# Kernel tuning notes

Hardware: AMD Instinct MI355X
Metric: run time of the kernel (lower is better)

The kernel has to match this reference:

```python
import jax, jax.numpy as jnp
import numpy as np

T, B, DIN, H, AA, L = 1024, 32, 256, 256, 21, 2


def setup_inputs() -> dict:
    key = jax.random.key(0)
    ks = jax.random.split(key, 8)
    scale = 0.05

    def rn(i, shape):
        return jax.random.normal(ks[i], shape, dtype=jnp.float32) * scale

    return {
        "x": jax.random.normal(ks[0], (B, T, DIN), dtype=jnp.float32),
        "hidden": jnp.zeros((2 * L, B, H), jnp.float32),  # accepted but unused, as in torch forward
        # layer 0: input DIN -> per-direction 4 chunks of H; layer 1: input 2H
        "w_l0": rn(1, (DIN, 2, 4, H)),
        "wc_l0": rn(2, (2, 2, H)),            # [dir, (v_f, v_r), H]
        "b_l0": jnp.zeros((2, 2, H), jnp.float32),  # [dir, (b_f, b_r), H]
        "w_l1": rn(3, (2 * H, 2, 4, H)),
        "wc_l1": rn(4, (2, 2, H)),
        "b_l1": jnp.zeros((2, 2, H), jnp.float32),
        "fc1_w": rn(5, (H, 2 * H)),
        "fc1_b": jnp.zeros((H,), jnp.float32),
        "lp_w": rn(6, (AA, H)),
        "lp_b": jnp.zeros((AA,), jnp.float32),
    }


def _sru_scan(u, vf, vr, bf, br):
    # u: (T, B, 4, H) with chunks [candidate, forget, reset, highway]
    def step(c, ut):
        f = jax.nn.sigmoid(ut[:, 1] + vf * c + bf)
        c2 = f * c + (1.0 - f) * ut[:, 0]
        r = jax.nn.sigmoid(ut[:, 2] + vr * c + br)
        h = r * c2 + (1.0 - r) * ut[:, 3]
        return c2, h

    c0 = jnp.zeros((u.shape[1], u.shape[-1]), u.dtype)
    _, hs = jax.lax.scan(step, c0, u)
    return hs  # (T, B, H)


def _sru_layer(x, w, wc, b):
    # x: (T, B, Din); w: (Din, 2, 4, H)
    U = jnp.einsum('tbd,dnkh->tbnkh', x, w)
    hf = _sru_scan(U[:, :, 0], wc[0, 0], wc[0, 1], b[0, 0], b[0, 1])
    hb = _sru_scan(U[::-1, :, 1], wc[1, 0], wc[1, 1], b[1, 0], b[1, 1])[::-1]
    return jnp.concatenate([hf, hb], axis=-1)  # (T, B, 2H)


def reference(x, hidden, w_l0, wc_l0, b_l0, w_l1, wc_l1, b_l1, fc1_w, fc1_b, lp_w, lp_b):
    h = jnp.transpose(x, (1, 0, 2))  # (T, B, DIN)
    h = _sru_layer(h, w_l0, wc_l0, b_l0)
    h = _sru_layer(h, w_l1, wc_l1, b_l1)
    h = jnp.transpose(h, (1, 0, 2))  # (B, T, 2H)
    h = h @ fc1_w.T + fc1_b
    logits = h @ lp_w.T + lp_b
    return jax.nn.log_softmax(logits, axis=-1)  # (B, T, AA)
```

## Files before the change

kernel.cpp:

```cpp
#include <hip/hip_runtime.h>
#include <hip/hip_bf16.h>

#define T_DIM 1024
#define B_DIM 32
#define DIN_DIM 256
#define H_DIM 256
#define AA_DIM 21
#define M_ROWS (B_DIM * T_DIM)

typedef __attribute__((ext_vector_type(8))) short bf16x8;
typedef __attribute__((ext_vector_type(4))) float f32x4;

typedef __attribute__((address_space(3))) void lds_void;
typedef const __attribute__((address_space(1))) void glb_void;

#define LOG2E_F 1.44269504088896340736f

__device__ __forceinline__ void gload_lds16(const void* g, void* l) {
    __builtin_amdgcn_global_load_lds((glb_void*)g, (lds_void*)l, 16, 0, 0);
}

__device__ __forceinline__ float b2f(unsigned short v) {
    unsigned u = ((unsigned)v) << 16;
    float f;
    __builtin_memcpy(&f, &u, 4);
    return f;
}

__device__ __forceinline__ unsigned short f2bu(float f) {
    __hip_bfloat16 h = __float2bfloat16(f);
    unsigned short u;
    __builtin_memcpy(&u, &h, 2);
    return u;
}

#define CVT_V0 2097152
#define CVT_N1 524288
#define CVT_N2 1048576
#define CVT_V3 32768
#define CVT_N4 8192
#define CVT_TOT (CVT_V0 + CVT_N1 + CVT_N2 + CVT_V3 + CVT_N4)
__global__ __launch_bounds__(256) void cvt_all(
    const float* __restrict__ x,  const float* __restrict__ w0,
    const float* __restrict__ w1, const float* __restrict__ fcw,
    const float* __restrict__ lpw,
    __hip_bfloat16* __restrict__ xb,  __hip_bfloat16* __restrict__ w0t,
    __hip_bfloat16* __restrict__ w1t, __hip_bfloat16* __restrict__ fcwb,
    __hip_bfloat16* __restrict__ lpwb)
{
    int i = blockIdx.x * 256 + threadIdx.x;
    if (i < CVT_V0) {
        float4 v = ((const float4*)x)[i];
        ushort4 o = { f2bu(v.x), f2bu(v.y), f2bu(v.z), f2bu(v.w) };
        ((ushort4*)xb)[i] = o;
        return;
    }
    i -= CVT_V0;
    if (i < CVT_N1) {
        int kk = i >> 11, rem = i & 2047;
        int dir = rem >> 10, k = (rem >> 8) & 3, h = rem & 255;
        w0t[(long)(dir * 1024 + h * 4 + k) * 256 + kk] = __float2bfloat16(w0[i]);
        return;
    }
    i -= CVT_N1;
    if (i < CVT_N2) {
        int kk = i >> 11, rem = i & 2047;
        int dir = rem >> 10, k = (rem >> 8) & 3, h = rem & 255;
        w1t[(long)(dir * 1024 + h * 4 + k) * 512 + kk] = __float2bfloat16(w1[i]);
        return;
    }
    i -= CVT_N2;
    if (i < CVT_V3) {
        float4 v = ((const float4*)fcw)[i];
        ushort4 o = { f2bu(v.x), f2bu(v.y), f2bu(v.z), f2bu(v.w) };
        ((ushort4*)fcwb)[i] = o;
        return;
    }
    i -= CVT_V3;
    if (i < CVT_N4) {
        int n = i >> 8, k = i & 255;
        lpwb[i] = __float2bfloat16(n < AA_DIM ? lpw[n * 256 + k] : 0.0f);
    }
}

template<int U2OUT>
__global__ __launch_bounds__(256) void gemm_bf16(
    const __hip_bfloat16* __restrict__ A,
    const __hip_bfloat16* __restrict__ Bt,
    const float* __restrict__ bias,
    __hip_bfloat16* __restrict__ C,
    int M, int N, int K, int nbShift)
{
    __shared__ __align__(16) char smb[32768];

    const int tid  = threadIdx.x;
    const int lane = tid & 63;
    const int wave = tid >> 6;
    const int wm = wave & 1;
    const int wn = wave >> 1;

    const int L   = blockIdx.x;
    const int s   = L >> 3;
    const int nb  = s & ((1 << nbShift) - 1);
    const int mb  = ((s >> nbShift) << 3) + (L & 7);
    const long n0 = (long)nb * 128;
    const long m0 = (long)mb * 128;

    f32x4 acc[4][4] = {};

    const int ldrow = lane >> 2;
    const int ldq   = lane & 3;
    const int gq    = ldq ^ ((ldrow >> 1) & 3);
    const int gkoff = gq * 8;

    const int fr = lane & 15;
    const int kq = lane >> 4;
    const int sw = (kq ^ ((fr >> 1) & 3)) * 16;

    for (int kb = 0; kb < K; kb += 64) {
        __syncthreads();
#pragma unroll
        for (int i = 0; i < 4; ++i) {
            const int cid = wave * 4 + i;
            const int rc  = cid >> 1;
            const int kh  = cid & 1;
            const long row = rc * 16 + ldrow;
            const int koff = kb + kh * 32 + gkoff;
            gload_lds16(A  + (m0 + row) * (long)K + koff,
                        smb + rc * 2048 + kh * 1024);
            gload_lds16(Bt + (n0 + row) * (long)K + koff,
                        smb + 16384 + rc * 2048 + kh * 1024);
        }
        __syncthreads();

#pragma unroll
        for (int ss = 0; ss < 2; ++ss) {
            bf16x8 af[4], bfv[4];
#pragma unroll
            for (int i = 0; i < 4; ++i) {
                af[i]  = *(const bf16x8*)(smb + (wm * 4 + i) * 2048 + ss * 1024 + fr * 64 + sw);
                bfv[i] = *(const bf16x8*)(smb + 16384 + (wn * 4 + i) * 2048 + ss * 1024 + fr * 64 + sw);
            }
#pragma unroll
            for (int i = 0; i < 4; ++i)
#pragma unroll
                for (int j = 0; j < 4; ++j)
                    acc[i][j] = __builtin_amdgcn_mfma_f32_16x16x32_bf16(
                        af[i], bfv[j], acc[i][j], 0, 0, 0);
        }
    }

    const int col_l = lane & 15;
    const int row_l = (lane >> 4) * 4;
    __hip_bfloat16* smC = (__hip_bfloat16*)smb;
#pragma unroll
    for (int p = 0; p < 2; ++p) {
        __syncthreads();
        if (wm == p) {
#pragma unroll
            for (int j = 0; j < 4; ++j) {
                const long gc = n0 + wn * 64 + j * 16 + col_l;
                const float bv = bias ? bias[gc] : 0.0f;
#pragma unroll
                for (int i = 0; i < 4; ++i)
#pragma unroll
                    for (int r = 0; r < 4; ++r)
                        smC[(i * 16 + row_l + r) * 132 + wn * 64 + j * 16 + col_l] =
                            __float2bfloat16(acc[i][j][r] + bv);
            }
        }
        __syncthreads();
        const int cb = (tid & 7) * 16;
#pragma unroll
        for (int s2 = 0; s2 < 2; ++s2) {
            const int rr = s2 * 32 + (tid >> 3);
            const long gr = m0 + p * 64 + rr;
            bf16x8 v0 = *(const bf16x8*)(smC + rr * 132 + cb);
            bf16x8 v1 = *(const bf16x8*)(smC + rr * 132 + cb + 8);
            if (U2OUT) {
                const int bI  = (int)(gr >> 10);
                const int t   = (int)(gr & 1023);
                const long gc0 = n0 + cb;
                const int dir = (int)(gc0 >> 10);
                const int hg  = ((int)gc0 >> 8) & 3;
                const int beta = bI * 8 + dir * 4 + hg;
                const long base = ((long)beta * 1024 + t) * 256 + (gc0 & 255);
                *(bf16x8*)(C + base)     = v0;
                *(bf16x8*)(C + base + 8) = v1;
            } else {
                *(bf16x8*)(C + gr * (long)N + n0 + cb)     = v0;
                *(bf16x8*)(C + gr * (long)N + n0 + cb + 8) = v1;
            }
        }
    }
}

#define SCAN_S 64
#define SCAN_NB (T_DIM / SCAN_S)
#define GRP 16

__device__ __forceinline__ float scan_step(
    uint2 u, float c, float nvf, float nvr, float nbf, float nbr,
    __hip_bfloat16* hq)
{
    float u0, u1, u2, u3;
    unsigned a0 = u.x << 16, a1 = u.x & 0xffff0000u;
    unsigned a2 = u.y << 16, a3 = u.y & 0xffff0000u;
    __builtin_memcpy(&u0, &a0, 4); __builtin_memcpy(&u1, &a1, 4);
    __builtin_memcpy(&u2, &a2, 4); __builtin_memcpy(&u3, &a3, 4);
    const float nf0 = __builtin_fmaf(-LOG2E_F, u1, nbf);
    const float nr0 = __builtin_fmaf(-LOG2E_F, u2, nbr);
    const float ef = __builtin_amdgcn_exp2f(__builtin_fmaf(nvf, c, nf0));
    const float er = __builtin_amdgcn_exp2f(__builtin_fmaf(nvr, c, nr0));
    const float f  = __builtin_amdgcn_rcpf(1.0f + ef);
    const float r  = __builtin_amdgcn_rcpf(1.0f + er);
    const float c2 = __builtin_fmaf(f, c - u0, u0);
    const float hv = __builtin_fmaf(r, c2 - u3, u3);
    *hq = __float2bfloat16(hv);
    return c2;
}

__global__ __launch_bounds__(256) void sru_scan(
    const __hip_bfloat16* __restrict__ U2,
    const float* __restrict__ wc,
    const float* __restrict__ bias,
    __hip_bfloat16* __restrict__ hout)
{
    __shared__ __align__(16) char lds[2 * SCAN_S * 512];
    const int tid  = threadIdx.x;
    const int wave = tid >> 6;
    const int lane = tid & 63;
    const int beta = blockIdx.x;
    const int b    = beta >> 3;
    const int dir  = (beta >> 2) & 1;
    const int hg   = beta & 3;
    const int h    = hg * 64 + lane;

    const char* gslice = (const char*)U2 + (size_t)beta * (1024 * 512);

    const float nvf = -LOG2E_F * wc[(dir * 2 + 0) * H_DIM + h];
    const float nvr = -LOG2E_F * wc[(dir * 2 + 1) * H_DIM + h];
    const float nbf = -LOG2E_F * bias[(dir * 2 + 0) * H_DIM + h];
    const float nbr = -LOG2E_F * bias[(dir * 2 + 1) * H_DIM + h];
    __hip_bfloat16* hp = hout + ((long)(b * 1024 + (dir ? 1023 : 0))) * 512 + dir * 256 + h;
    const long hstep = dir ? -512L : 512L;
    float c = 0.0f;

    const int plane = lane & 31;

    if (wave > 0) {
        for (int p = wave - 1; p < SCAN_S / 2; p += 3) {
            const int sl = 2 * p + (lane >> 5);
            const int t  = dir ? (1023 - sl) : sl;
            gload_lds16(gslice + (size_t)t * 512 + plane * 16, lds + p * 1024);
        }
    }
    __syncthreads();

    for (int bat = 0; bat < SCAN_NB; ++bat) {
        if (wave > 0) {
            if (bat + 1 < SCAN_NB) {
                char* halfN = lds + ((bat + 1) & 1) * (SCAN_S * 512);
                const int tb = (bat + 1) * SCAN_S;
                for (int p = wave - 1; p < SCAN_S / 2; p += 3) {
                    const int sl = tb + 2 * p + (lane >> 5);
                    const int t  = dir ? (1023 - sl) : sl;
                    gload_lds16(gslice + (size_t)t * 512 + plane * 16,
                                halfN + p * 1024);
                }
            }
        } else {
            const char* half = lds + (bat & 1) * (SCAN_S * 512);
            __hip_bfloat16* hq = hp + (long)(bat * SCAN_S) * hstep;
            uint2 qa[GRP], qb[GRP];
#pragma unroll
            for (int j = 0; j < GRP; ++j)
                qa[j] = *(const uint2*)(half + (0 * GRP + j) * 512 + (lane << 3));
#pragma unroll
            for (int j = 0; j < GRP; ++j)
                qb[j] = *(const uint2*)(half + (1 * GRP + j) * 512 + (lane << 3));
#pragma unroll
            for (int j = 0; j < GRP; ++j)
                c = scan_step(qa[j], c, nvf, nvr, nbf, nbr, hq + (long)j * hstep);
#pragma unroll
            for (int j = 0; j < GRP; ++j)
                qa[j] = *(const uint2*)(half + (2 * GRP + j) * 512 + (lane << 3));
#pragma unroll
            for (int j = 0; j < GRP; ++j)
                c = scan_step(qb[j], c, nvf, nvr, nbf, nbr, hq + (long)(GRP + j) * hstep);
#pragma unroll
            for (int j = 0; j < GRP; ++j)
                qb[j] = *(const uint2*)(half + (3 * GRP + j) * 512 + (lane << 3));
#pragma unroll
            for (int j = 0; j < GRP; ++j)
                c = scan_step(qa[j], c, nvf, nvr, nbf, nbr, hq + (long)(2 * GRP + j) * hstep);
#pragma unroll
            for (int j = 0; j < GRP; ++j)
                c = scan_step(qb[j], c, nvf, nvr, nbf, nbr, hq + (long)(3 * GRP + j) * hstep);
        }
        __syncthreads();
    }
}

__global__ __launch_bounds__(256) void logits_mfma(
    const __hip_bfloat16* __restrict__ fc,
    const __hip_bfloat16* __restrict__ lpwb,
    const float* __restrict__ lpb,
    float* __restrict__ out)
{
    __shared__ __align__(16) char smb[25088];
    const int tid  = threadIdx.x;
    const int lane = tid & 63;
    const int wave = tid >> 6;
    const long m0  = (long)blockIdx.x * 128;

    for (int idx = tid; idx < 32 * 32; idx += 256) {
        const int rw = idx >> 5, sl = idx & 31;
        *(bf16x8*)(smb + rw * 528 + sl * 16) =
            *(const bf16x8*)(lpwb + rw * 256 + sl * 8);
    }

    const int ldrow = lane >> 2;
    const int ldq   = lane & 3;
    const int gq    = ldq ^ ((ldrow >> 1) & 3);
    const int gkoff = gq * 8;

    const int fr = lane & 15;
    const int kq = lane >> 4;
    const int sw = (kq ^ ((fr >> 1) & 3)) * 16;

    f32x4 acc[2][2] = {};
    for (int kc = 0; kc < 8; ++kc) {
        __syncthreads();
#pragma unroll
        for (int i = 0; i < 2; ++i) {
            const int rc = wave * 2 + i;
            gload_lds16(fc + (m0 + rc * 16 + ldrow) * 256 + kc * 32 + gkoff,
                        smb + 16896 + rc * 1024);
        }
        __syncthreads();
        bf16x8 af[2], bfv[2];
#pragma unroll
        for (int i = 0; i < 2; ++i)
            af[i] = *(const bf16x8*)(smb + 16896 + (wave * 2 + i) * 1024 + fr * 64 + sw);
#pragma unroll
        for (int j = 0; j < 2; ++j)
            bfv[j] = *(const bf16x8*)(smb + (j * 16 + fr) * 528 + kc * 64 + kq * 16);
#pragma unroll
        for (int i = 0; i < 2; ++i)
#pragma unroll
            for (int j = 0; j < 2; ++j)
                acc[i][j] = __builtin_amdgcn_mfma_f32_16x16x32_bf16(
                    af[i], bfv[j], acc[i][j], 0, 0, 0);
    }

    __syncthreads();
    float* smC = (float*)smb;
    const int col_l = lane & 15;
    const int row_l = (lane >> 4) * 4;
#pragma unroll
    for (int j = 0; j < 2; ++j) {
        const int gc = j * 16 + col_l;
        const float bv = (gc < AA_DIM) ? lpb[gc] : 0.0f;
#pragma unroll
        for (int i = 0; i < 2; ++i)
#pragma unroll
            for (int r = 0; r < 4; ++r)
                smC[(wave * 32 + i * 16 + row_l + r) * 36 + gc] = acc[i][j][r] + bv;
    }
    __syncthreads();
    if (tid < 128) {
        const float* rowp = smC + tid * 36;
        float m = rowp[0];
#pragma unroll
        for (int a = 1; a < AA_DIM; ++a) m = fmaxf(m, rowp[a]);
        float s = 0.0f;
#pragma unroll
        for (int a = 0; a < AA_DIM; ++a) s += __expf(rowp[a] - m);
        const float lse = __logf(s) + m;
        float* op = out + (m0 + tid) * AA_DIM;
#pragma unroll
        for (int a = 0; a < AA_DIM; ++a) op[a] = rowp[a] - lse;
    }
}

extern "C" void kernel_launch(void* const* d_in, const int* in_sizes, int n_in,
                              void* d_out, int out_size, void* d_ws, size_t ws_size,
                              hipStream_t stream)
{
    const float* x     = (const float*)d_in[0];
    const float* w_l0  = (const float*)d_in[2];
    const float* wc_l0 = (const float*)d_in[3];
    const float* b_l0  = (const float*)d_in[4];
    const float* w_l1  = (const float*)d_in[5];
    const float* wc_l1 = (const float*)d_in[6];
    const float* b_l1  = (const float*)d_in[7];
    const float* fc1_w = (const float*)d_in[8];
    const float* fc1_b = (const float*)d_in[9];
    const float* lp_w  = (const float*)d_in[10];
    const float* lp_b  = (const float*)d_in[11];
    float* out = (float*)d_out;

    char* ws = (char*)d_ws;
    __hip_bfloat16* U      = (__hip_bfloat16*)(ws);
    __hip_bfloat16* h0b    = (__hip_bfloat16*)(ws + 134217728);
    __hip_bfloat16* h1b    = (__hip_bfloat16*)(ws + 167772160);
    __hip_bfloat16* xb     = (__hip_bfloat16*)(ws + 201326592);
    __hip_bfloat16* fcob   = xb;
    __hip_bfloat16* w0t    = (__hip_bfloat16*)(ws + 218103808);
    __hip_bfloat16* w1t    = (__hip_bfloat16*)(ws + 219152384);
    __hip_bfloat16* fc1wb  = (__hip_bfloat16*)(ws + 221249536);
    __hip_bfloat16* lpwb   = (__hip_bfloat16*)(ws + 221511680);

    cvt_all<<<(CVT_TOT + 255) / 256, 256, 0, stream>>>(
        x, w_l0, w_l1, fc1_w, lp_w, xb, w0t, w1t, fc1wb, lpwb);

    gemm_bf16<1><<<4096, 256, 0, stream>>>(
        xb, w0t, nullptr, U, M_ROWS, 2048, DIN_DIM, 4);
    sru_scan<<<256, 256, 0, stream>>>(U, wc_l0, b_l0, h0b);
    gemm_bf16<1><<<4096, 256, 0, stream>>>(
        h0b, w1t, nullptr, U, M_ROWS, 2048, 512, 4);
    sru_scan<<<256, 256, 0, stream>>>(U, wc_l1, b_l1, h1b);
    gemm_bf16<0><<<512, 256, 0, stream>>>(
        h1b, fc1wb, fc1_b, fcob, M_ROWS, 256, 512, 1);
    logits_mfma<<<M_ROWS / 128, 256, 0, stream>>>(fcob, lpwb, lp_b, out);
}
```

Measured before the change: 402.2 us.

## Add 256x256-tile double-buffered MFMA GEMM for SRU input projections

Replaces the two large U-projection GEMMs with a new 512-thread kernel that computes 256x256 output tiles. It double-buffers K-tiles in 128KB of LDS through direct global-to-LDS loads and interleaves LDS fragment reads with MFMA bursts under barriers and raised wave priority. Larger tiles raise arithmetic intensity and cut redundant A/B loads. The cost is high LDS and register use per block, which limits occupancy, and the epilogue now writes the permuted U layout through an LDS staging buffer.

```diff
diff --git a/kernel.cpp b/kernel.cpp
--- a/kernel.cpp
+++ b/kernel.cpp
@@ -80,6 +80,176 @@
     if (i < CVT_N4) {
         int n = i >> 8, k = i & 255;
         lpwb[i] = __float2bfloat16(n < AA_DIM ? lpw[n * 256 + k] : 0.0f);
+    }
+}
+
+__device__ __forceinline__ void stage_tile256(
+    const __hip_bfloat16* __restrict__ A,
+    const __hip_bfloat16* __restrict__ Bt,
+    char* buf, long m0, long n0, int K, int kb,
+    int wave, int ldrow, int gkoff)
+{
+#pragma unroll
+    for (int i = 0; i < 4; ++i) {
+        const int cid = wave * 4 + i;
+        const int rc  = cid >> 1;
+        const int kh  = cid & 1;
+        const long row = rc * 16 + ldrow;
+        const int koff = kb + kh * 32 + gkoff;
+        gload_lds16(A  + (m0 + row) * (long)K + koff,
+                    buf + rc * 2048 + kh * 1024);
+        gload_lds16(Bt + (n0 + row) * (long)K + koff,
+                    buf + 32768 + rc * 2048 + kh * 1024);
+    }
+}
+
+#define MFMA16(d, a, b) d = __builtin_amdgcn_mfma_f32_16x16x32_bf16(a, b, d, 0, 0, 0)
+
+__global__ __launch_bounds__(512, 2) void gemm256_u2(
+    const __hip_bfloat16* __restrict__ A,
+    const __hip_bfloat16* __restrict__ Bt,
+    __hip_bfloat16* __restrict__ C,
+    int K, int nbShift)
+{
+    __shared__ __align__(16) char smb[131072];
+
+    const int tid  = threadIdx.x;
+    const int lane = tid & 63;
+    const int wave = tid >> 6;
+    const int wm   = wave >> 2;
+    const int wn   = wave & 3;
+
+    const int L  = blockIdx.x;
+    const int s  = L >> 3;
+    const int nb = s & ((1 << nbShift) - 1);
+    const int mb = ((s >> nbShift) << 3) + (L & 7);
+    const long n0 = (long)nb * 256;
+    const long m0 = (long)mb * 256;
+
+    const int ldrow = lane >> 2;
+    const int ldq   = lane & 3;
+    const int gq    = ldq ^ ((ldrow >> 1) & 3);
+    const int gkoff = gq * 8;
+
+    const int fr = lane & 15;
+    const int kq = lane >> 4;
+    const int sw = (kq ^ ((fr >> 1) & 3)) * 16;
+
+    f32x4 acc[8][4] = {};
+    const int NT = K >> 6;
+
+    stage_tile256(A, Bt, smb,         m0, n0, K, 0,  wave, ldrow, gkoff);
+    __builtin_amdgcn_sched_barrier(0);
+    stage_tile256(A, Bt, smb + 65536, m0, n0, K, 64, wave, ldrow, gkoff);
+    asm volatile("s_waitcnt vmcnt(8)" ::: "memory");
+    __builtin_amdgcn_s_barrier();
+
+    for (int kt = 0; kt < NT; ++kt) {
+        char* rb = smb + (kt & 1) * 65536;
+        const char* Ab = rb + (wm * 8) * 2048;
+        const char* Bb = rb + 32768 + (wn * 4) * 2048;
+        bf16x8 a0[4], a1[4], bv[4];
+
+#pragma unroll
+        for (int i = 0; i < 4; ++i) {
+            a0[i] = *(const bf16x8*)(Ab + i * 2048 + fr * 64 + sw);
+            bv[i] = *(const bf16x8*)(Bb + i * 2048 + fr * 64 + sw);
+        }
+        __builtin_amdgcn_s_barrier();
+        __builtin_amdgcn_s_setprio(1);
+#pragma unroll
+        for (int i = 0; i < 4; ++i)
+#pragma unroll
+            for (int j = 0; j < 4; ++j)
+                MFMA16(acc[i][j], a0[i], bv[j]);
+        __builtin_amdgcn_s_setprio(0);
+        __builtin_amdgcn_s_barrier();
+
+#pragma unroll
+        for (int i = 0; i < 4; ++i)
+            a1[i] = *(const bf16x8*)(Ab + (4 + i) * 2048 + fr * 64 + sw);
+        __builtin_amdgcn_s_barrier();
+        __builtin_amdgcn_s_setprio(1);
+#pragma unroll
+        for (int i = 0; i < 4; ++i)
+#pragma unroll
+            for (int j = 0; j < 4; ++j)
+                MFMA16(acc[4 + i][j], a1[i], bv[j]);
+        __builtin_amdgcn_s_setprio(0);
+        __builtin_amdgcn_s_barrier();
+
+#pragma unroll
+        for (int i = 0; i < 4; ++i) {
+            a0[i] = *(const bf16x8*)(Ab + i * 2048 + 1024 + fr * 64 + sw);
+            bv[i] = *(const bf16x8*)(Bb + i * 2048 + 1024 + fr * 64 + sw);
+        }
+        __builtin_amdgcn_s_barrier();
+        __builtin_amdgcn_s_setprio(1);
+#pragma unroll
+        for (int i = 0; i < 4; ++i)
+#pragma unroll
+            for (int j = 0; j < 4; ++j)
+                MFMA16(acc[i][j], a0[i], bv[j]);
+        __builtin_amdgcn_s_setprio(0);
+        __builtin_amdgcn_s_barrier();
+
+#pragma unroll
+        for (int i = 0; i < 4; ++i)
+            a1[i] = *(const bf16x8*)(Ab + (4 + i) * 2048 + 1024 + fr * 64 + sw);
+        __builtin_amdgcn_s_barrier();
+        __builtin_amdgcn_s_setprio(1);
+#pragma unroll
+        for (int i = 0; i < 4; ++i)
+#pragma unroll
+            for (int j = 0; j < 4; ++j)
+                MFMA16(acc[4 + i][j], a1[i], bv[j]);
+        __builtin_amdgcn_s_setprio(0);
+        __builtin_amdgcn_s_barrier();
+
+        __builtin_amdgcn_sched_barrier(0);
+        if (kt + 2 < NT) {
+            stage_tile256(A, Bt, rb, m0, n0, K, (kt + 2) * 64,
+                          wave, ldrow, gkoff);
+            asm volatile("s_waitcnt vmcnt(8)" ::: "memory");
+        } else if (kt + 1 < NT) {
+            asm volatile("s_waitcnt vmcnt(0)" ::: "memory");
+        }
+        __builtin_amdgcn_s_barrier();
+    }
+
+    const int col_l = lane & 15;
+    const int row_l = (lane >> 4) * 4;
+    __hip_bfloat16* smC = (__hip_bfloat16*)smb;
+    const int chunk = tid & 31;
+    const int rbase = tid >> 5;
+#pragma unroll
+    for (int p = 0; p < 2; ++p) {
+        __syncthreads();
+        if (wm == p) {
+#pragma unroll
+            for (int i = 0; i < 8; ++i)
+#pragma unroll
+                for (int j = 0; j < 4; ++j)
+#pragma unroll
+                    for (int r = 0; r < 4; ++r)
+                        smC[(i * 16 + row_l + r) * 264 + wn * 64 + j * 16 + col_l] =
+                            __float2bfloat16(acc[i][j][r]);
+        }
+        __syncthreads();
+#pragma unroll
+        for (int it = 0; it < 8; ++it) {
+            const int rr = it * 16 + rbase;
+            bf16x8 v = *(const bf16x8*)(smC + rr * 264 + chunk * 8);
+            const long gr  = m0 + p * 128 + rr;
+            const long gc0 = n0 + chunk * 8;
+            const int bI  = (int)(gr >> 10);
+            const int t   = (int)(gr & 1023);
+            const int dir = (int)(gc0 >> 10);
+            const int hg  = ((int)gc0 >> 8) & 3;
+            const int beta = bI * 8 + dir * 4 + hg;
+            const long base = ((long)beta * 1024 + t) * 256 + ((int)gc0 & 255);
+            *(bf16x8*)(C + base) = v;
+        }
     }
 }
 
@@ -415,11 +585,9 @@
     cvt_all<<<(CVT_TOT + 255) / 256, 256, 0, stream>>>(
         x, w_l0, w_l1, fc1_w, lp_w, xb, w0t, w1t, fc1wb, lpwb);
 
-    gemm_bf16<1><<<4096, 256, 0, stream>>>(
-        xb, w0t, nullptr, U, M_ROWS, 2048, DIN_DIM, 4);
+    gemm256_u2<<<1024, 512, 0, stream>>>(xb, w0t, U, DIN_DIM, 3);
     sru_scan<<<256, 256, 0, stream>>>(U, wc_l0, b_l0, h0b);
-    gemm_bf16<1><<<4096, 256, 0, stream>>>(
-        h0b, w1t, nullptr, U, M_ROWS, 2048, 512, 4);
+    gemm256_u2<<<1024, 512, 0, stream>>>(h0b, w1t, U, 512, 3);
     sru_scan<<<256, 256, 0, stream>>>(U, wc_l1, b_l1, h1b);
     gemm_bf16<0><<<512, 256, 0, stream>>>(
         h1b, fc1wb, fc1_b, fcob, M_ROWS, 256, 512, 1);
```

After: 389.1 us. 1.03x faster.

## Fuse SRU input projection GEMM with recurrent scan in warp-specialized kernel

Applied to the files above, without the earlier changes.

Replaces the separate projection GEMM and scan kernels for each layer with one kernel. Eight producer waves compute 64-timestep chunks of U with MFMA into double-buffered LDS, and one consumer wave runs the recurrence from LDS. This removes the round trip of the large U intermediate through global memory and overlaps the matmul with the sequential scan. The cost is that the GEMM now runs on only 256 blocks with one block per CU, and correctness depends on hand-written barrier and waitcnt synchronization.

```diff
diff --git a/kernel.cpp b/kernel.cpp
--- a/kernel.cpp
+++ b/kernel.cpp
@@ -18,13 +18,6 @@
 
 __device__ __forceinline__ void gload_lds16(const void* g, void* l) {
     __builtin_amdgcn_global_load_lds((glb_void*)g, (lds_void*)l, 16, 0, 0);
-}
-
-__device__ __forceinline__ float b2f(unsigned short v) {
-    unsigned u = ((unsigned)v) << 16;
-    float f;
-    __builtin_memcpy(&f, &u, 4);
-    return f;
 }
 
 __device__ __forceinline__ unsigned short f2bu(float f) {
@@ -83,6 +76,203 @@
     }
 }
 
+#define MFMA16(d, a, b) d = __builtin_amdgcn_mfma_f32_16x16x32_bf16(a, b, d, 0, 0, 0)
+
+__device__ __forceinline__ float scan_step(
+    uint2 u, float c, float nvf, float nvr, float nbf, float nbr,
+    __hip_bfloat16* hq)
+{
+    float u0, u1, u2, u3;
+    unsigned a0 = u.x << 16, a1 = u.x & 0xffff0000u;
+    unsigned a2 = u.y << 16, a3 = u.y & 0xffff0000u;
+    __builtin_memcpy(&u0, &a0, 4); __builtin_memcpy(&u1, &a1, 4);
+    __builtin_memcpy(&u2, &a2, 4); __builtin_memcpy(&u3, &a3, 4);
+    const float nf0 = __builtin_fmaf(-LOG2E_F, u1, nbf);
+    const float nr0 = __builtin_fmaf(-LOG2E_F, u2, nbr);
+    const float ef = __builtin_amdgcn_exp2f(__builtin_fmaf(nvf, c, nf0));
+    const float er = __builtin_amdgcn_exp2f(__builtin_fmaf(nvr, c, nr0));
+    const float f  = __builtin_amdgcn_rcpf(1.0f + ef);
+    const float r  = __builtin_amdgcn_rcpf(1.0f + er);
+    const float c2 = __builtin_fmaf(f, c - u0, u0);
+    const float hv = __builtin_fmaf(r, c2 - u3, u3);
+    *hq = __float2bfloat16(hv);
+    return c2;
+}
+
+#define CH_S 64
+#define NCH (T_DIM / CH_S)
+#define USTRIDE 520
+#define UBUF_SZ (CH_S * USTRIDE)
+#define BOFF (2 * UBUF_SZ)
+#define LDS_TOT (BOFF + 8 * 2 * 4096)
+
+template<int K>
+__global__ __launch_bounds__(576, 1) void fused_sru(
+    const __hip_bfloat16* __restrict__ A,
+    const __hip_bfloat16* __restrict__ Bt,
+    const float* __restrict__ wc,
+    const float* __restrict__ bias,
+    __hip_bfloat16* __restrict__ hout)
+{
+    constexpr int NK = K / 64;
+    __shared__ __align__(16) char lds[LDS_TOT];
+
+    const int tid  = threadIdx.x;
+    const int wave = tid >> 6;
+    const int lane = tid & 63;
+    const int beta = blockIdx.x;
+    const int b    = beta >> 3;
+    const int dir  = (beta >> 2) & 1;
+    const int hg   = beta & 3;
+
+    if (wave < 8) {
+        const int fr = lane & 15, kq = lane >> 4;
+        const int sw = (kq ^ ((fr >> 1) & 3)) * 16;
+        const int ldrow = lane >> 2, ldq = lane & 3;
+        const int gq = ldq ^ ((ldrow >> 1) & 3);
+        const int gkoff = gq * 8;
+        char* bb = lds + BOFF + wave * 8192;
+        const int nb0 = dir * 1024 + hg * 256;
+        const long arowB = (long)b * 1024;
+        const long browW = (long)(nb0 + wave * 32);
+        const int row_l = (lane >> 4) * 4;
+        const int col_l = lane & 15;
+
+        bf16x8 ar[2][8];
+
+        {
+            const long arow0 = arowB + (dir ? (1024 - CH_S) : 0);
+#pragma unroll
+            for (int g = 0; g < 2; ++g) {
+#pragma unroll
+                for (int i = 0; i < 4; ++i)
+#pragma unroll
+                    for (int kh = 0; kh < 2; ++kh)
+                        ar[g][i * 2 + kh] = *(const bf16x8*)(A +
+                            (arow0 + i * 16 + fr) * (long)K + g * 64 + kh * 32 + kq * 8);
+#pragma unroll
+                for (int j = 0; j < 2; ++j)
+#pragma unroll
+                    for (int kh = 0; kh < 2; ++kh)
+                        gload_lds16(Bt + (browW + j * 16 + ldrow) * (long)K +
+                                        g * 64 + kh * 32 + gkoff,
+                                    bb + g * 4096 + j * 2048 + kh * 1024);
+                __builtin_amdgcn_sched_barrier(0);
+            }
+        }
+
+        for (int c = 0; c < NCH; ++c) {
+            const long arow_c = arowB + (dir ? (long)(1024 - (c + 1) * CH_S)
+                                             : (long)(c * CH_S));
+            const long arow_n = arowB + (dir ? (long)(1024 - (c + 2) * CH_S)
+                                             : (long)((c + 1) * CH_S));
+            const bool haveN = (c + 1 < NCH);
+            f32x4 acc[4][2] = {};
+            __hip_bfloat16* ub = (__hip_bfloat16*)(lds + (c & 1) * UBUF_SZ);
+
+#pragma unroll
+            for (int ks = 0; ks < NK; ++ks) {
+                if (c == NCH - 1 && ks == NK - 1)
+                    asm volatile("s_waitcnt vmcnt(0)" ::: "memory");
+                else
+                    asm volatile("s_waitcnt vmcnt(12)" ::: "memory");
+
+                bf16x8 bfr[4];
+#pragma unroll
+                for (int j = 0; j < 2; ++j)
+#pragma unroll
+                    for (int kh = 0; kh < 2; ++kh)
+                        bfr[j * 2 + kh] = *(const bf16x8*)(bb + (ks & 1) * 4096 +
+                                           j * 2048 + kh * 1024 + fr * 64 + sw);
+#pragma unroll
+                for (int kh = 0; kh < 2; ++kh)
+#pragma unroll
+                    for (int i = 0; i < 4; ++i)
+#pragma unroll
+                        for (int j = 0; j < 2; ++j)
+                            MFMA16(acc[i][j], ar[ks & 1][i * 2 + kh], bfr[j * 2 + kh]);
+
+                const bool wrap = (ks + 2 >= NK);
+                const int  nks  = wrap ? (ks + 2 - NK) : (ks + 2);
+                const long arw  = wrap ? arow_n : arow_c;
+                if (!wrap || haveN) {
+#pragma unroll
+                    for (int i = 0; i < 4; ++i)
+#pragma unroll
+                        for (int kh = 0; kh < 2; ++kh)
+                            ar[ks & 1][i * 2 + kh] = *(const bf16x8*)(A +
+                                (arw + i * 16 + fr) * (long)K + nks * 64 + kh * 32 + kq * 8);
+#pragma unroll
+                    for (int j = 0; j < 2; ++j)
+#pragma unroll
+                        for (int kh = 0; kh < 2; ++kh)
+                            gload_lds16(Bt + (browW + j * 16 + ldrow) * (long)K +
+                                            nks * 64 + kh * 32 + gkoff,
+                                        bb + (ks & 1) * 4096 + j * 2048 + kh * 1024);
+                }
+            }
+
+#pragma unroll
+            for (int i = 0; i < 4; ++i)
+#pragma unroll
+                for (int j = 0; j < 2; ++j)
+#pragma unroll
+                    for (int r = 0; r < 4; ++r)
+                        ub[(i * 16 + row_l + r) * (USTRIDE / 2) +
+                           wave * 32 + j * 16 + col_l] =
+                            __float2bfloat16(acc[i][j][r]);
+
+            asm volatile("s_waitcnt lgkmcnt(0)" ::: "memory");
+            __builtin_amdgcn_s_barrier();
+            asm volatile("" ::: "memory");
+            __builtin_amdgcn_sched_barrier(0);
+        }
+    } else {
+        const int h = hg * 64 + lane;
+        const float nvf = -LOG2E_F * wc[(dir * 2 + 0) * H_DIM + h];
+        const float nvr = -LOG2E_F * wc[(dir * 2 + 1) * H_DIM + h];
+        const float nbf = -LOG2E_F * bias[(dir * 2 + 0) * H_DIM + h];
+        const float nbr = -LOG2E_F * bias[(dir * 2 + 1) * H_DIM + h];
+        __hip_bfloat16* hp = hout + ((long)(b * 1024 + (dir ? 1023 : 0))) * 512 +
+                             dir * 256 + h;
+        const long hstep = dir ? -512L : 512L;
+        float cc = 0.0f;
+
+        for (int c = 0; c < NCH; ++c) {
+            __builtin_amdgcn_s_barrier();
+            asm volatile("" ::: "memory");
+            __builtin_amdgcn_sched_barrier(0);
+            const char* ub = lds + (c & 1) * UBUF_SZ;
+            __hip_bfloat16* hq = hp + (long)(c * CH_S) * hstep;
+            uint2 qa[16], qb[16];
+#pragma unroll
+            for (int j = 0; j < 16; ++j)
+                qa[j] = *(const uint2*)(ub + (dir ? (63 - j) : j) * USTRIDE + (lane << 3));
+#pragma unroll
+            for (int j = 0; j < 16; ++j)
+                qb[j] = *(const uint2*)(ub + (dir ? (47 - j) : (16 + j)) * USTRIDE + (lane << 3));
+#pragma unroll
+            for (int j = 0; j < 16; ++j)
+                cc = scan_step(qa[j], cc, nvf, nvr, nbf, nbr, hq + (long)j * hstep);
+#pragma unroll
+            for (int j = 0; j < 16; ++j)
+                qa[j] = *(const uint2*)(ub + (dir ? (31 - j) : (32 + j)) * USTRIDE + (lane << 3));
+#pragma unroll
+            for (int j = 0; j < 16; ++j)
+                cc = scan_step(qb[j], cc, nvf, nvr, nbf, nbr, hq + (long)(16 + j) * hstep);
+#pragma unroll
+            for (int j = 0; j < 16; ++j)
+                qb[j] = *(const uint2*)(ub + (dir ? (15 - j) : (48 + j)) * USTRIDE + (lane << 3));
+#pragma unroll
+            for (int j = 0; j < 16; ++j)
+                cc = scan_step(qa[j], cc, nvf, nvr, nbf, nbr, hq + (long)(32 + j) * hstep);
+#pragma unroll
+            for (int j = 0; j < 16; ++j)
+                cc = scan_step(qb[j], cc, nvf, nvr, nbf, nbr, hq + (long)(48 + j) * hstep);
+        }
+    }
+}
+
 template<int U2OUT>
 __global__ __launch_bounds__(256) void gemm_bf16(
     const __hip_bfloat16* __restrict__ A,
@@ -195,113 +385,6 @@
     }
 }
 
-#define SCAN_S 64
-#define SCAN_NB (T_DIM / SCAN_S)
-#define GRP 16
-
-__device__ __forceinline__ float scan_step(
-    uint2 u, float c, float nvf, float nvr, float nbf, float nbr,
-    __hip_bfloat16* hq)
-{
-    float u0, u1, u2, u3;
-    unsigned a0 = u.x << 16, a1 = u.x & 0xffff0000u;
-    unsigned a2 = u.y << 16, a3 = u.y & 0xffff0000u;
-    __builtin_memcpy(&u0, &a0, 4); __builtin_memcpy(&u1, &a1, 4);
-    __builtin_memcpy(&u2, &a2, 4); __builtin_memcpy(&u3, &a3, 4);
-    const float nf0 = __builtin_fmaf(-LOG2E_F, u1, nbf);
-    const float nr0 = __builtin_fmaf(-LOG2E_F, u2, nbr);
-    const float ef = __builtin_amdgcn_exp2f(__builtin_fmaf(nvf, c, nf0));
-    const float er = __builtin_amdgcn_exp2f(__builtin_fmaf(nvr, c, nr0));
-    const float f  = __builtin_amdgcn_rcpf(1.0f + ef);
-    const float r  = __builtin_amdgcn_rcpf(1.0f + er);
-    const float c2 = __builtin_fmaf(f, c - u0, u0);
-    const float hv = __builtin_fmaf(r, c2 - u3, u3);
-    *hq = __float2bfloat16(hv);
-    return c2;
-}
-
-__global__ __launch_bounds__(256) void sru_scan(
-    const __hip_bfloat16* __restrict__ U2,
-    const float* __restrict__ wc,
-    const float* __restrict__ bias,
-    __hip_bfloat16* __restrict__ hout)
-{
-    __shared__ __align__(16) char lds[2 * SCAN_S * 512];
-    const int tid  = threadIdx.x;
-    const int wave = tid >> 6;
-    const int lane = tid & 63;
-    const int beta = blockIdx.x;
-    const int b    = beta >> 3;
-    const int dir  = (beta >> 2) & 1;
-    const int hg   = beta & 3;
-    const int h    = hg * 64 + lane;
-
-    const char* gslice = (const char*)U2 + (size_t)beta * (1024 * 512);
-
-    const float nvf = -LOG2E_F * wc[(dir * 2 + 0) * H_DIM + h];
-    const float nvr = -LOG2E_F * wc[(dir * 2 + 1) * H_DIM + h];
-    const float nbf = -LOG2E_F * bias[(dir * 2 + 0) * H_DIM + h];
-    const float nbr = -LOG2E_F * bias[(dir * 2 + 1) * H_DIM + h];
-    __hip_bfloat16* hp = hout + ((long)(b * 1024 + (dir ? 1023 : 0))) * 512 + dir * 256 + h;
-    const long hstep = dir ? -512L : 512L;
-    float c = 0.0f;
-
-    const int plane = lane & 31;
-
-    if (wave > 0) {
-        for (int p = wave - 1; p < SCAN_S / 2; p += 3) {
-            const int sl = 2 * p + (lane >> 5);
-            const int t  = dir ? (1023 - sl) : sl;
-            gload_lds16(gslice + (size_t)t * 512 + plane * 16, lds + p * 1024);
-        }
-    }
-    __syncthreads();
-
-    for (int bat = 0; bat < SCAN_NB; ++bat) {
-        if (wave > 0) {
-            if (bat + 1 < SCAN_NB) {
-                char* halfN = lds + ((bat + 1) & 1) * (SCAN_S * 512);
-                const int tb = (bat + 1) * SCAN_S;
-                for (int p = wave - 1; p < SCAN_S / 2; p += 3) {
-                    const int sl = tb + 2 * p + (lane >> 5);
-                    const int t  = dir ? (1023 - sl) : sl;
-                    gload_lds16(gslice + (size_t)t * 512 + plane * 16,
-                                halfN + p * 1024);
-                }
-            }
-        } else {
-            const char* half = lds + (bat & 1) * (SCAN_S * 512);
-            __hip_bfloat16* hq = hp + (long)(bat * SCAN_S) * hstep;
-            uint2 qa[GRP], qb[GRP];
-#pragma unroll
-            for (int j = 0; j < GRP; ++j)
-                qa[j] = *(const uint2*)(half + (0 * GRP + j) * 512 + (lane << 3));
-#pragma unroll
-            for (int j = 0; j < GRP; ++j)
-                qb[j] = *(const uint2*)(half + (1 * GRP + j) * 512 + (lane << 3));
-#pragma unroll
-            for (int j = 0; j < GRP; ++j)
-                c = scan_step(qa[j], c, nvf, nvr, nbf, nbr, hq + (long)j * hstep);
-#pragma unroll
-            for (int j = 0; j < GRP; ++j)
-                qa[j] = *(const uint2*)(half + (2 * GRP + j) * 512 + (lane << 3));
-#pragma unroll
-            for (int j = 0; j < GRP; ++j)
-                c = scan_step(qb[j], c, nvf, nvr, nbf, nbr, hq + (long)(GRP + j) * hstep);
-#pragma unroll
-            for (int j = 0; j < GRP; ++j)
-                qb[j] = *(const uint2*)(half + (3 * GRP + j) * 512 + (lane << 3));
-#pragma unroll
-            for (int j = 0; j < GRP; ++j)
-                c = scan_step(qa[j], c, nvf, nvr, nbf, nbr, hq + (long)(2 * GRP + j) * hstep);
-#pragma unroll
-            for (int j = 0; j < GRP; ++j)
-                c = scan_step(qb[j], c, nvf, nvr, nbf, nbr, hq + (long)(3 * GRP + j) * hstep);
-        }
-        __syncthreads();
-    }
-}
-
 __global__ __launch_bounds__(256) void logits_mfma(
     const __hip_bfloat16* __restrict__ fc,
     const __hip_bfloat16* __restrict__ lpwb,
@@ -402,7 +485,6 @@
     float* out = (float*)d_out;
 
     char* ws = (char*)d_ws;
-    __hip_bfloat16* U      = (__hip_bfloat16*)(ws);
     __hip_bfloat16* h0b    = (__hip_bfloat16*)(ws + 134217728);
     __hip_bfloat16* h1b    = (__hip_bfloat16*)(ws + 167772160);
     __hip_bfloat16* xb     = (__hip_bfloat16*)(ws + 201326592);
@@ -415,12 +497,9 @@
     cvt_all<<<(CVT_TOT + 255) / 256, 256, 0, stream>>>(
         x, w_l0, w_l1, fc1_w, lp_w, xb, w0t, w1t, fc1wb, lpwb);
 
-    gemm_bf16<1><<<4096, 256, 0, stream>>>(
-        xb, w0t, nullptr, U, M_ROWS, 2048, DIN_DIM, 4);
-    sru_scan<<<256, 256, 0, stream>>>(U, wc_l0, b_l0, h0b);
-    gemm_bf16<1><<<4096, 256, 0, stream>>>(
-        h0b, w1t, nullptr, U, M_ROWS, 2048, 512, 4);
-    sru_scan<<<256, 256, 0, stream>>>(U, wc_l1, b_l1, h1b);
+    fused_sru<256><<<256, 576, 0, stream>>>(xb,  w0t, wc_l0, b_l0, h0b);
+    fused_sru<512><<<256, 576, 0, stream>>>(h0b, w1t, wc_l1, b_l1, h1b);
+
     gemm_bf16<0><<<512, 256, 0, stream>>>(
         h1b, fc1wb, fc1_b, fcob, M_ROWS, 256, 512, 1);
     logits_mfma<<<M_ROWS / 128, 256, 0, stream>>>(fcob, lpwb, lp_b, out);
```

Result: slower. 566.7 us (+40.9%).

## Double-buffer LDS tiles in bf16 GEMM to overlap global loads with MFMA

Applied to the files above, without the earlier changes.

The GEMM kernel now keeps two 32 KB LDS stages. It issues the async global-to-LDS loads for tile k+1 before computing tile k, and uses a manual vmcnt wait with raw s_barrier in place of two __syncthreads per iteration. It also raises wave priority around the MFMA block and requests two blocks per CU through launch bounds. This aims to hide global load latency behind matrix math, at the cost of doubling LDS use to 64 KB per block, which may limit occupancy. The K loops are short (4 or 8 tiles), so the prologue load is exposed for a relatively large share of each block.

```diff
diff --git a/kernel.cpp b/kernel.cpp
--- a/kernel.cpp
+++ b/kernel.cpp
@@ -18,13 +18,6 @@
 
 __device__ __forceinline__ void gload_lds16(const void* g, void* l) {
     __builtin_amdgcn_global_load_lds((glb_void*)g, (lds_void*)l, 16, 0, 0);
-}
-
-__device__ __forceinline__ float b2f(unsigned short v) {
-    unsigned u = ((unsigned)v) << 16;
-    float f;
-    __builtin_memcpy(&f, &u, 4);
-    return f;
 }
 
 __device__ __forceinline__ unsigned short f2bu(float f) {
@@ -83,15 +76,17 @@
     }
 }
 
+#define MFMA16(d, a, b) d = __builtin_amdgcn_mfma_f32_16x16x32_bf16(a, b, d, 0, 0, 0)
+
 template<int U2OUT>
-__global__ __launch_bounds__(256) void gemm_bf16(
+__global__ __launch_bounds__(256, 2) void gemm128_db(
     const __hip_bfloat16* __restrict__ A,
     const __hip_bfloat16* __restrict__ Bt,
     const float* __restrict__ bias,
     __hip_bfloat16* __restrict__ C,
     int M, int N, int K, int nbShift)
 {
-    __shared__ __align__(16) char smb[32768];
+    __shared__ __align__(16) char smb[65536];
 
     const int tid  = threadIdx.x;
     const int lane = tid & 63;
@@ -117,38 +112,59 @@
     const int kq = lane >> 4;
     const int sw = (kq ^ ((fr >> 1) & 3)) * 16;
 
-    for (int kb = 0; kb < K; kb += 64) {
-        __syncthreads();
-#pragma unroll
-        for (int i = 0; i < 4; ++i) {
-            const int cid = wave * 4 + i;
-            const int rc  = cid >> 1;
-            const int kh  = cid & 1;
-            const long row = rc * 16 + ldrow;
-            const int koff = kb + kh * 32 + gkoff;
-            gload_lds16(A  + (m0 + row) * (long)K + koff,
-                        smb + rc * 2048 + kh * 1024);
-            gload_lds16(Bt + (n0 + row) * (long)K + koff,
-                        smb + 16384 + rc * 2048 + kh * 1024);
-        }
-        __syncthreads();
+    const int NT = K >> 6;
+
+#define STAGE128(BUF, KB)                                                   \
+    do {                                                                    \
+        _Pragma("unroll")                                                   \
+        for (int i = 0; i < 4; ++i) {                                       \
+            const int cid = wave * 4 + i;                                   \
+            const int rc  = cid >> 1;                                       \
+            const int kh  = cid & 1;                                        \
+            const long row = rc * 16 + ldrow;                               \
+            const int koff = (KB) + kh * 32 + gkoff;                        \
+            gload_lds16(A  + (m0 + row) * (long)K + koff,                   \
+                        (BUF) + rc * 2048 + kh * 1024);                     \
+            gload_lds16(Bt + (n0 + row) * (long)K + koff,                   \
+                        (BUF) + 16384 + rc * 2048 + kh * 1024);             \
+        }                                                                   \
+    } while (0)
+
+    STAGE128(smb, 0);
+
+    for (int kt = 0; kt < NT; ++kt) {
+        char* cur = smb + (kt & 1) * 32768;
+        char* nxt = smb + ((kt + 1) & 1) * 32768;
+
+        __builtin_amdgcn_sched_barrier(0);
+        if (kt + 1 < NT) {
+            STAGE128(nxt, (kt + 1) * 64);
+            __builtin_amdgcn_sched_barrier(0);
+            asm volatile("s_waitcnt vmcnt(8)" ::: "memory");
+        } else {
+            asm volatile("s_waitcnt vmcnt(0)" ::: "memory");
+        }
+        __builtin_amdgcn_s_barrier();
 
 #pragma unroll
         for (int ss = 0; ss < 2; ++ss) {
             bf16x8 af[4], bfv[4];
 #pragma unroll
             for (int i = 0; i < 4; ++i) {
-                af[i]  = *(const bf16x8*)(smb + (wm * 4 + i) * 2048 + ss * 1024 + fr * 64 + sw);
-                bfv[i] = *(const bf16x8*)(smb + 16384 + (wn * 4 + i) * 2048 + ss * 1024 + fr * 64 + sw);
+                af[i]  = *(const bf16x8*)(cur + (wm * 4 + i) * 2048 + ss * 1024 + fr * 64 + sw);
+                bfv[i] = *(const bf16x8*)(cur + 16384 + (wn * 4 + i) * 2048 + ss * 1024 + fr * 64 + sw);
             }
+            __builtin_amdgcn_s_setprio(1);
 #pragma unroll
             for (int i = 0; i < 4; ++i)
 #pragma unroll
                 for (int j = 0; j < 4; ++j)
-                    acc[i][j] = __builtin_amdgcn_mfma_f32_16x16x32_bf16(
-                        af[i], bfv[j], acc[i][j], 0, 0, 0);
-        }
-    }
+                    MFMA16(acc[i][j], af[i], bfv[j]);
+            __builtin_amdgcn_s_setprio(0);
+        }
+        __builtin_amdgcn_s_barrier();
+    }
+#undef STAGE128
 
     const int col_l = lane & 15;
     const int row_l = (lane >> 4) * 4;
@@ -415,13 +431,13 @@
     cvt_all<<<(CVT_TOT + 255) / 256, 256, 0, stream>>>(
         x, w_l0, w_l1, fc1_w, lp_w, xb, w0t, w1t, fc1wb, lpwb);
 
-    gemm_bf16<1><<<4096, 256, 0, stream>>>(
+    gemm128_db<1><<<4096, 256, 0, stream>>>(
         xb, w0t, nullptr, U, M_ROWS, 2048, DIN_DIM, 4);
     sru_scan<<<256, 256, 0, stream>>>(U, wc_l0, b_l0, h0b);
-    gemm_bf16<1><<<4096, 256, 0, stream>>>(
+    gemm128_db<1><<<4096, 256, 0, stream>>>(
         h0b, w1t, nullptr, U, M_ROWS, 2048, 512, 4);
     sru_scan<<<256, 256, 0, stream>>>(U, wc_l1, b_l1, h1b);
-    gemm_bf16<0><<<512, 256, 0, stream>>>(
+    gemm128_db<0><<<512, 256, 0, stream>>>(
         h1b, fc1wb, fc1_b, fcob, M_ROWS, 256, 512, 1);
     logits_mfma<<<M_ROWS / 128, 256, 0, stream>>>(fcob, lpwb, lp_b, out);
 }
```

After: 397.0 us. About the same (-1.3%).
